# Kernel optimization log

Hardware: AMD Instinct MI355X
Metric: run time of the kernel (lower is better)

The kernel has to match this reference:

```python
import jax, jax.numpy as jnp
import numpy as np

B, L = 2, 256
H, W = 256, 128
FLAT = H * W              # 32768
D_MODEL = 1024
D_INNER = 2 * D_MODEL     # 2048
D_STATE = 16
D_CONV = 4
DT_RANK = D_MODEL // 16   # 64


def _rmsnorm(x, w, eps=1e-5):
    return x * jax.lax.rsqrt(jnp.mean(x * x, axis=-1, keepdims=True) + eps) * w


def _selective_scan(dA, dBu, C):
    # dA, dBu: (B, L, D_INNER, D_STATE); C: (B, L, D_STATE)
    def step(h, inp):
        a, bu, c = inp
        h = a * h + bu
        return h, jnp.einsum('bdn,bn->bd', h, c)
    h0 = jnp.zeros((dA.shape[0], dA.shape[2], dA.shape[3]), dA.dtype)
    _, ys = jax.lax.scan(step, h0, (jnp.swapaxes(dA, 0, 1), jnp.swapaxes(dBu, 0, 1), jnp.swapaxes(C, 0, 1)))
    return jnp.swapaxes(ys, 0, 1)  # (B, L, D_INNER)


def _mamba_block(x, norm_w, in_proj_w, conv_w, conv_b, x_proj_w, dt_proj_w, dt_proj_b, A_log, D_skip, out_proj_w):
    xn = _rmsnorm(x, norm_w)
    xz = xn @ in_proj_w.T                        # (B, L, 2*D_INNER)
    u, z = jnp.split(xz, 2, axis=-1)
    # causal depthwise conv over the sequence dim
    u = jax.lax.conv_general_dilated(u, conv_w, (1,), [(D_CONV - 1, 0)],
                                     dimension_numbers=('NWC', 'WIO', 'NWC'),
                                     feature_group_count=D_INNER) + conv_b
    u = jax.nn.silu(u)
    dbc = u @ x_proj_w.T                         # (B, L, DT_RANK + 2*D_STATE)
    dt_r, Bm, Cm = jnp.split(dbc, [DT_RANK, DT_RANK + D_STATE], axis=-1)
    dt = jax.nn.softplus(dt_r @ dt_proj_w.T + dt_proj_b)  # (B, L, D_INNER)
    A = -jnp.exp(A_log)                          # (D_INNER, D_STATE)
    dA = jnp.exp(dt[..., None] * A)              # (B, L, D_INNER, D_STATE)
    dBu = (dt * u)[..., None] * Bm[:, :, None, :]
    y = _selective_scan(dA, dBu, Cm) + D_skip * u
    y = y * jax.nn.silu(z)
    return x + y @ out_proj_w.T


def setup_inputs():
    key = jax.random.key(0)
    ks = jax.random.split(key, 12)
    g = lambda i, shape, sc: jax.random.normal(ks[i], shape, dtype=jnp.float32) * sc
    return {
        'x': (jax.random.uniform(ks[0], (B, L, H, W)) < 0.1).astype(jnp.float32),
        'enc_w': g(1, (D_MODEL, FLAT), 0.005),
        'enc_b': jnp.zeros((D_MODEL,), jnp.float32),
        'dec_w': g(2, (FLAT, D_MODEL), 0.02),
        'dec_b': jnp.zeros((FLAT,), jnp.float32),
        'norm_w': jnp.ones((D_MODEL,), jnp.float32),
        'in_proj_w': g(3, (2 * D_INNER, D_MODEL), 0.02),
        'conv_w': g(4, (D_CONV, 1, D_INNER), 0.2),
        'conv_b': jnp.zeros((D_INNER,), jnp.float32),
        'x_proj_w': g(5, (DT_RANK + 2 * D_STATE, D_INNER), 0.02),
        'dt_proj_w': g(6, (D_INNER, DT_RANK), 0.1),
        'dt_proj_b': jnp.full((D_INNER,), -2.0, jnp.float32),
        'A_log': jnp.log(jnp.tile(jnp.arange(1, D_STATE + 1, dtype=jnp.float32), (D_INNER, 1))),
        'D_skip': jnp.ones((D_INNER,), jnp.float32),
        'out_proj_w': g(7, (D_MODEL, D_INNER), 0.02),
    }


def reference(x, enc_w, enc_b, dec_w, dec_b, norm_w, in_proj_w, conv_w, conv_b,
              x_proj_w, dt_proj_w, dt_proj_b, A_log, D_skip, out_proj_w):
    b, l = x.shape[:2]
    lat = x.reshape(b, l, FLAT) @ enc_w.T + enc_b          # frozen encoder
    h = _mamba_block(lat, norm_w, in_proj_w, conv_w, conv_b, x_proj_w,
                     dt_proj_w, dt_proj_b, A_log, D_skip, out_proj_w)
    probs = jax.nn.sigmoid(h @ dec_w.T + dec_b)            # frozen decoder + sigmoid
    return probs.reshape(b, l, H, W)[:, :-1]
```

## Files before the change

### kernel.cpp

```cpp
#include <hip/hip_runtime.h>
#include <math.h>
#include <stdint.h>

#define BB 2
#define LL 256
#define FLAT 32768
#define DM 1024
#define DI 2048
#define DS 16
#define DTR 64
#define ML (BB*LL)

#define EPI_NONE 0
#define EPI_BIAS 1
#define EPI_SOFTPLUS 2
#define EPI_DEC 4

typedef __attribute__((ext_vector_type(8))) short bf16x8;
typedef __attribute__((ext_vector_type(4))) float f32x4;
typedef __attribute__((ext_vector_type(8))) unsigned short u16x8;
typedef __attribute__((ext_vector_type(4))) unsigned short u16x4;

__device__ __forceinline__ float sigmoid_f(float x) { return 1.0f / (1.0f + __expf(-x)); }

__device__ __forceinline__ unsigned short f2bf(float f) {
    unsigned u = __float_as_uint(f);
    u += 0x7fffu + ((u >> 16) & 1u);
    return (unsigned short)(u >> 16);
}

__device__ __forceinline__ unsigned cvt_pk_bf16(float a, float b) {
    unsigned r;
    asm("v_cvt_pk_bf16_f32 %0, %1, %2" : "=v"(r) : "v"(a), "v"(b));
    return r;
}

__device__ __forceinline__ void gld_lds16(const void* g, void* l) {
    __builtin_amdgcn_global_load_lds(
        (const __attribute__((address_space(1))) unsigned int*)g,
        (__attribute__((address_space(3))) unsigned int*)l, 16, 0, 0);
}

__global__ __launch_bounds__(256) void cvt_bf16_k(
    const float* __restrict__ in, unsigned short* __restrict__ out, int n8)
{
    const int i = blockIdx.x * 256 + threadIdx.x;
    if (i >= n8) return;
    const float4 a = ((const float4*)in)[2 * i];
    const float4 b = ((const float4*)in)[2 * i + 1];
    u16x8 r;
    r[0] = f2bf(a.x); r[1] = f2bf(a.y); r[2] = f2bf(a.z); r[3] = f2bf(a.w);
    r[4] = f2bf(b.x); r[5] = f2bf(b.y); r[6] = f2bf(b.z); r[7] = f2bf(b.w);
    ((u16x8*)out)[i] = r;
}

template<int EPI, bool SPLIT>
__global__ __launch_bounds__(256) void gemm_db(
    const unsigned short* __restrict__ A, const unsigned short* __restrict__ B,
    float* __restrict__ C, int M, int N, int K, int lda, int ldb, int kChunk,
    const float* __restrict__ bias)
{
    __shared__ __align__(16) char lds[65536];

    const int t  = threadIdx.x;
    const int w  = t >> 6;
    const int l  = t & 63;
    const int m0 = blockIdx.x * 128;
    const int n0 = blockIdx.y * 128;
    const int wr = w >> 1, wc = w & 1;

    int kb = 0, ke = K;
    float* Cout = C;
    if (SPLIT) { kb = blockIdx.z * kChunk; ke = kb + kChunk;
                 Cout = C + (size_t)blockIdx.z * M * N; }

    const int srow0 = w * 32 + (l >> 3);
    const int ssub  = l & 7;

    f32x4 acc[4][4];
#pragma unroll
    for (int i = 0; i < 4; ++i)
#pragma unroll
        for (int j = 0; j < 4; ++j) acc[i][j] = (f32x4){0.f, 0.f, 0.f, 0.f};

    const int lr = l & 15, h = l >> 4;

    auto STAGE = [&](int p, int kt) {
#pragma unroll
        for (int q = 0; q < 4; ++q) {
            const int row = srow0 + q * 8;
            gld_lds16(A + (size_t)(m0 + row) * lda + kt + ((ssub ^ (row & 7)) << 3),
                      lds + p * 32768 + w * 4096 + q * 1024);
        }
#pragma unroll
        for (int q = 0; q < 4; ++q) {
            const int row = srow0 + q * 8;
            gld_lds16(B + (size_t)(n0 + row) * ldb + kt + ((ssub ^ (row & 7)) << 3),
                      lds + p * 32768 + 16384 + w * 4096 + q * 1024);
        }
    };

    STAGE(0, kb);
    asm volatile("s_waitcnt vmcnt(0)" ::: "memory");
    __builtin_amdgcn_s_barrier();

    const int nt = (ke - kb) >> 6;
    int cur = 0;
    for (int tt = 0; tt < nt; ++tt) {
        if (tt + 1 < nt) STAGE(cur ^ 1, kb + ((tt + 1) << 6));
        const char* la = lds + cur * 32768;
        const char* lb = la + 16384;
#pragma unroll
        for (int ks = 0; ks < 2; ++ks) {
            bf16x8 af[4], bfr[4];
#pragma unroll
            for (int i = 0; i < 4; ++i) {
                const int r = wr * 64 + i * 16 + lr;
                const int sub = (ks * 4 + h) ^ (r & 7);
                af[i] = *(const bf16x8*)(la + r * 128 + sub * 16);
            }
#pragma unroll
            for (int j = 0; j < 4; ++j) {
                const int c = wc * 64 + j * 16 + lr;
                const int sub = (ks * 4 + h) ^ (c & 7);
                bfr[j] = *(const bf16x8*)(lb + c * 128 + sub * 16);
            }
#pragma unroll
            for (int i = 0; i < 4; ++i)
#pragma unroll
                for (int j = 0; j < 4; ++j)
                    acc[i][j] = __builtin_amdgcn_mfma_f32_16x16x32_bf16(
                        af[i], bfr[j], acc[i][j], 0, 0, 0);
        }
        asm volatile("s_waitcnt vmcnt(0)" ::: "memory");
        __builtin_amdgcn_s_barrier();
        cur ^= 1;
    }

#pragma unroll
    for (int i = 0; i < 4; ++i)
#pragma unroll
        for (int j = 0; j < 4; ++j)
#pragma unroll
            for (int rg = 0; rg < 4; ++rg) {
                const int row = m0 + wr * 64 + i * 16 + h * 4 + rg;
                const int col = n0 + wc * 64 + j * 16 + lr;
                float v = acc[i][j][rg];
                if (SPLIT || EPI == EPI_NONE) {
                    Cout[(size_t)row * N + col] = v;
                } else if (EPI == EPI_DEC) {
                    v = sigmoid_f(v + bias[col]);
                    const int b = row >> 8, ll = row & 255;
                    if (ll < 255) Cout[(((size_t)(b * 255 + ll)) << 15) + col] = v;
                }
            }
}

template<int EPI, bool SPLIT, bool BF32>
__global__ __launch_bounds__(256) void gemm_bf16(
    const unsigned short* __restrict__ A, const void* __restrict__ Bv,
    float* __restrict__ C, int M, int N, int K, int lda, int ldb, int kChunk,
    const float* __restrict__ bias)
{
    __shared__ __align__(16) char lds[BF32 ? 49152 : 32768];

    const float*          Bf = (const float*)Bv;
    const unsigned short* Bh = (const unsigned short*)Bv;

    const int t  = threadIdx.x;
    const int w  = t >> 6;
    const int l  = t & 63;
    const int m0 = blockIdx.x * 128;
    const int n0 = blockIdx.y * 128;
    const int wr = w >> 1, wc = w & 1;

    int kb = 0, ke = K;
    float* Cout = C;
    if (SPLIT) { kb = blockIdx.z * kChunk; ke = kb + kChunk;
                 Cout = C + (size_t)blockIdx.z * M * N; }

    const int srow0 = w * 32 + (l >> 3);
    const int ssub  = l & 7;
    const int brow0 = w * 32 + (l >> 4);
    const int bgl   = l & 15;

    f32x4 acc[4][4];
#pragma unroll
    for (int i = 0; i < 4; ++i)
#pragma unroll
        for (int j = 0; j < 4; ++j) acc[i][j] = (f32x4){0.f, 0.f, 0.f, 0.f};

    const int lr = l & 15, h = l >> 4;

    for (int kt = kb; kt < ke; kt += 64) {
#pragma unroll
        for (int q = 0; q < 4; ++q) {
            const int row = srow0 + q * 8;
            gld_lds16(A + (size_t)(m0 + row) * lda + kt + ((ssub ^ (row & 7)) << 3),
                      lds + w * 4096 + q * 1024);
        }
        if (BF32) {
#pragma unroll
            for (int q = 0; q < 8; ++q) {
                const int row = brow0 + q * 4;
                gld_lds16(Bf + (size_t)(n0 + row) * ldb + kt + ((bgl ^ (row & 15)) << 2),
                          lds + 16384 + w * 8192 + q * 1024);
            }
        } else {
#pragma unroll
            for (int q = 0; q < 4; ++q) {
                const int row = srow0 + q * 8;
                gld_lds16(Bh + (size_t)(n0 + row) * ldb + kt + ((ssub ^ (row & 7)) << 3),
                          lds + 16384 + w * 4096 + q * 1024);
            }
        }
        __syncthreads();

#pragma unroll
        for (int ks = 0; ks < 2; ++ks) {
            bf16x8 af[4], bfr[4];
#pragma unroll
            for (int i = 0; i < 4; ++i) {
                const int r = wr * 64 + i * 16 + lr;
                const int sub = (ks * 4 + h) ^ (r & 7);
                af[i] = *(const bf16x8*)(lds + r * 128 + sub * 16);
            }
#pragma unroll
            for (int j = 0; j < 4; ++j) {
                const int c = wc * 64 + j * 16 + lr;
                if (BF32) {
                    const int g0 = (2 * (ks * 4 + h))     ^ (c & 15);
                    const int g1 = (2 * (ks * 4 + h) + 1) ^ (c & 15);
                    const f32x4 v0 = *(const f32x4*)(lds + 16384 + c * 256 + g0 * 16);
                    const f32x4 v1 = *(const f32x4*)(lds + 16384 + c * 256 + g1 * 16);
                    union { unsigned u[4]; bf16x8 v; } cv;
                    cv.u[0] = cvt_pk_bf16(v0[0], v0[1]);
                    cv.u[1] = cvt_pk_bf16(v0[2], v0[3]);
                    cv.u[2] = cvt_pk_bf16(v1[0], v1[1]);
                    cv.u[3] = cvt_pk_bf16(v1[2], v1[3]);
                    bfr[j] = cv.v;
                } else {
                    const int sub = (ks * 4 + h) ^ (c & 7);
                    bfr[j] = *(const bf16x8*)(lds + 16384 + c * 128 + sub * 16);
                }
            }
#pragma unroll
            for (int i = 0; i < 4; ++i)
#pragma unroll
                for (int j = 0; j < 4; ++j)
                    acc[i][j] = __builtin_amdgcn_mfma_f32_16x16x32_bf16(
                        af[i], bfr[j], acc[i][j], 0, 0, 0);
        }
        __syncthreads();
    }

#pragma unroll
    for (int i = 0; i < 4; ++i)
#pragma unroll
        for (int j = 0; j < 4; ++j)
#pragma unroll
            for (int rg = 0; rg < 4; ++rg) {
                const int row = m0 + wr * 64 + i * 16 + h * 4 + rg;
                const int col = n0 + wc * 64 + j * 16 + lr;
                float v = acc[i][j][rg];
                if (SPLIT || EPI == EPI_NONE) {
                    Cout[(size_t)row * N + col] = v;
                } else if (EPI == EPI_DEC) {
                    v = sigmoid_f(v + bias[col]);
                    const int b = row >> 8, ll = row & 255;
                    if (ll < 255) Cout[(((size_t)(b * 255 + ll)) << 15) + col] = v;
                }
            }
}

template<int EPI, bool SPLIT>
__global__ __launch_bounds__(256) void gemm_nt(
    const float* __restrict__ A, const float* __restrict__ B,
    float* __restrict__ C, int M, int N, int K, int lda, int ldb,
    int kChunk, const float* __restrict__ bias)
{
    __shared__ float As[32][64];
    __shared__ float Bs[32][64];

    const int m0 = blockIdx.x * 64;
    const int n0 = blockIdx.y * 64;
    const int t  = threadIdx.x;

    int kb = 0, ke = K;
    float* Cout = C;
    if (SPLIT) { kb = blockIdx.z * kChunk; ke = kb + kChunk; Cout = C + (size_t)blockIdx.z * M * N; }

    const int lrow = t >> 3;
    const int lcol = (t & 7) << 2;

    float acc[4][4];
#pragma unroll
    for (int i = 0; i < 4; ++i)
#pragma unroll
        for (int j = 0; j < 4; ++j) acc[i][j] = 0.0f;

    const int tx = t & 15, ty = t >> 4;

    for (int k = kb; k < ke; k += 32) {
#pragma unroll
        for (int i = 0; i < 2; ++i) {
            const int row = lrow + i * 32;
            float4 av = *(const float4*)&A[(m0 + row) * lda + k + lcol];
            As[lcol + 0][row] = av.x; As[lcol + 1][row] = av.y;
            As[lcol + 2][row] = av.z; As[lcol + 3][row] = av.w;
            const int nn = n0 + row;
            float4 bv = make_float4(0.f, 0.f, 0.f, 0.f);
            if (nn < N) bv = *(const float4*)&B[nn * ldb + k + lcol];
            Bs[lcol + 0][row] = bv.x; Bs[lcol + 1][row] = bv.y;
            Bs[lcol + 2][row] = bv.z; Bs[lcol + 3][row] = bv.w;
        }
        __syncthreads();
#pragma unroll
        for (int kk = 0; kk < 32; ++kk) {
            float4 a4 = *(const float4*)&As[kk][ty << 2];
            float4 b4 = *(const float4*)&Bs[kk][tx << 2];
            const float a[4] = { a4.x, a4.y, a4.z, a4.w };
            const float b[4] = { b4.x, b4.y, b4.z, b4.w };
#pragma unroll
            for (int i = 0; i < 4; ++i)
#pragma unroll
                for (int j = 0; j < 4; ++j)
                    acc[i][j] = fmaf(a[i], b[j], acc[i][j]);
        }
        __syncthreads();
    }

#pragma unroll
    for (int i = 0; i < 4; ++i) {
        const int m = m0 + (ty << 2) + i;
#pragma unroll
        for (int j = 0; j < 4; ++j) {
            const int n = n0 + (tx << 2) + j;
            if (n >= N) continue;
            float v = acc[i][j];
            if (SPLIT || EPI == EPI_NONE) {
                Cout[m * N + n] = v;
            } else if (EPI == EPI_SOFTPLUS) {
                v += bias[n];
                Cout[m * N + n] = fmaxf(v, 0.0f) + log1pf(__expf(-fabsf(v)));
            }
        }
    }
}

template<int EPI>
__global__ __launch_bounds__(256) void splitk_reduce(
    const float* __restrict__ part, float* __restrict__ C,
    int MN, int N, int S, const float* __restrict__ bias)
{
    const int i = blockIdx.x * 256 + threadIdx.x;
    if (i >= MN) return;
    float s = 0.0f;
    for (int j = 0; j < S; ++j) s += part[(size_t)j * MN + i];
    if (EPI == EPI_BIAS) s += bias[i % N];
    C[i] = s;
}

__global__ __launch_bounds__(256) void splitk_reduce_resid_bf16(
    const float* __restrict__ part, const float* __restrict__ resid,
    unsigned short* __restrict__ outb, int MN, int S)
{
    const int i = blockIdx.x * 256 + threadIdx.x;
    if (i >= MN) return;
    float s = 0.0f;
    for (int j = 0; j < S; ++j) s += part[(size_t)j * MN + i];
    outb[i] = f2bf(s + resid[i]);
}

__global__ __launch_bounds__(256) void rmsnorm_k(
    const float* __restrict__ x, const float* __restrict__ w,
    unsigned short* __restrict__ o)
{
    const int row = blockIdx.x;
    const int t = threadIdx.x;
    const float* xr = x + row * DM;
    float4 xv = *(const float4*)&xr[t * 4];
    float ss = xv.x * xv.x + xv.y * xv.y + xv.z * xv.z + xv.w * xv.w;
#pragma unroll
    for (int off = 32; off > 0; off >>= 1) ss += __shfl_xor(ss, off);
    __shared__ float red[4];
    if ((t & 63) == 0) red[t >> 6] = ss;
    __syncthreads();
    const float tot = red[0] + red[1] + red[2] + red[3];
    const float scale = rsqrtf(tot * (1.0f / DM) + 1e-5f);
    float4 wv = *(const float4*)&w[t * 4];
    u16x4 ov;
    ov[0] = f2bf(xv.x * scale * wv.x); ov[1] = f2bf(xv.y * scale * wv.y);
    ov[2] = f2bf(xv.z * scale * wv.z); ov[3] = f2bf(xv.w * scale * wv.w);
    *(u16x4*)&o[row * DM + t * 4] = ov;
}

__global__ __launch_bounds__(256) void conv_silu_k(
    const float* __restrict__ xz, const float* __restrict__ cw,
    const float* __restrict__ cb, float* __restrict__ u)
{
    const int idx = blockIdx.x * 256 + threadIdx.x;
    if (idx >= ML * DI) return;
    const int d  = idx & (DI - 1);
    const int bl = idx >> 11;
    const int l  = bl & (LL - 1);
    float s = cb[d];
#pragma unroll
    for (int w = 0; w < 4; ++w) {
        const int ls = l - 3 + w;
        if (ls >= 0) s = fmaf(xz[(bl - 3 + w) * (2 * DI) + d], cw[w * DI + d], s);
    }
    u[idx] = s * sigmoid_f(s);
}

__global__ __launch_bounds__(256) void scan_k(
    const float* __restrict__ dt, const float* __restrict__ u,
    const float* __restrict__ xz, const float* __restrict__ dbc,
    const float* __restrict__ A_log, const float* __restrict__ Dskip,
    unsigned short* __restrict__ y)
{
    const int t = blockIdx.x * 256 + threadIdx.x;
    const int n  = t & (DS - 1);
    const int ch = t >> 4;
    const int d  = ch & (DI - 1);
    const int b  = ch >> 11;
    const float a  = -__expf(A_log[d * DS + n]);
    const float Dv = Dskip[d];
    float h = 0.0f;
    const int rbase = b * LL;

    for (int l0 = 0; l0 < LL; l0 += 8) {
        float dtv[8], uv[8], Bv[8], Cv[8], zv[8];
#pragma unroll
        for (int s = 0; s < 8; ++s) {
            const int r = rbase + l0 + s;
            dtv[s] = dt[r * DI + d];
            uv[s]  = u[r * DI + d];
            Bv[s]  = dbc[r * 96 + DTR + n];
            Cv[s]  = dbc[r * 96 + DTR + DS + n];
            zv[s]  = xz[r * (2 * DI) + DI + d];
        }
        float p[8];
#pragma unroll
        for (int s = 0; s < 8; ++s) {
            const float dA = __expf(dtv[s] * a);
            h = fmaf(dA, h, dtv[s] * uv[s] * Bv[s]);
            p[s] = h * Cv[s];
        }
#pragma unroll
        for (int s = 0; s < 8; ++s) p[s] += __shfl_xor(p[s], 1);
#pragma unroll
        for (int s = 0; s < 8; ++s) p[s] += __shfl_xor(p[s], 2);
#pragma unroll
        for (int s = 0; s < 8; ++s) p[s] += __shfl_xor(p[s], 4);
#pragma unroll
        for (int s = 0; s < 8; ++s) p[s] += __shfl_xor(p[s], 8);
        if (n == 0) {
#pragma unroll
            for (int s = 0; s < 8; ++s) {
                const int r = rbase + l0 + s;
                const float yy = fmaf(Dv, uv[s], p[s]);
                y[r * DI + d] = f2bf(yy * zv[s] * sigmoid_f(zv[s]));
            }
        }
    }
}

extern "C" void kernel_launch(void* const* d_in, const int* in_sizes, int n_in,
                              void* d_out, int out_size, void* d_ws, size_t ws_size,
                              hipStream_t stream)
{
    const float* x        = (const float*)d_in[0];
    const float* enc_w    = (const float*)d_in[1];
    const float* enc_b    = (const float*)d_in[2];
    const float* dec_w    = (const float*)d_in[3];
    const float* dec_b    = (const float*)d_in[4];
    const float* norm_w   = (const float*)d_in[5];
    const float* in_proj  = (const float*)d_in[6];
    const float* conv_w   = (const float*)d_in[7];
    const float* conv_b   = (const float*)d_in[8];
    const float* x_proj   = (const float*)d_in[9];
    const float* dt_projw = (const float*)d_in[10];
    const float* dt_projb = (const float*)d_in[11];
    const float* A_log    = (const float*)d_in[12];
    const float* D_skip   = (const float*)d_in[13];
    const float* out_proj = (const float*)d_in[14];
    float* out = (float*)d_out;
    (void)in_sizes; (void)n_in; (void)out_size; (void)ws_size;

    char* wsb = (char*)d_ws;
    unsigned short* wbf = (unsigned short*)(wsb);
    float* part = (float*)(wsb + 67108864);
    float* lat  = (float*)(wsb + 100663296);
    float* dt   = (float*)(wsb + 102760448);
    char* S0 = wsb + 106954752;
    unsigned short* xbf    = (unsigned short*)(S0);
    unsigned short* xnbf   = (unsigned short*)(S0);
    unsigned short* ybf    = (unsigned short*)(S0 + 1048576);
    unsigned short* houtbf = (unsigned short*)(S0 + 3145728);
    float* xz  = (float*)(S0 + 4194304);
    float* u   = (float*)(S0 + 12582912);
    float* dbc = (float*)(S0 + 16777216);

    cvt_bf16_k<<<(FLAT * ML / 8) / 256, 256, 0, stream>>>(x, xbf, FLAT * ML / 8);
    cvt_bf16_k<<<(DM * FLAT / 8) / 256, 256, 0, stream>>>(enc_w, wbf, DM * FLAT / 8);

    {
        dim3 g(ML / 128, DM / 128, 16);
        gemm_db<EPI_NONE, true><<<g, 256, 0, stream>>>(
            xbf, wbf, part, ML, DM, FLAT, FLAT, FLAT, FLAT / 16, nullptr);
        splitk_reduce<EPI_BIAS><<<(ML * DM) / 256, 256, 0, stream>>>(part, lat, ML * DM, DM, 16, enc_b);
    }

    rmsnorm_k<<<ML, 256, 0, stream>>>(lat, norm_w, xnbf);

    {
        dim3 g(ML / 128, (2 * DI) / 128);
        gemm_bf16<EPI_NONE, false, true><<<g, 256, 0, stream>>>(
            xnbf, in_proj, xz, ML, 2 * DI, DM, DM, DM, 0, nullptr);
    }

    conv_silu_k<<<(ML * DI) / 256, 256, 0, stream>>>(xz, conv_w, conv_b, u);

    {
        dim3 g(ML / 64, 2, 16);
        gemm_nt<EPI_NONE, true><<<g, 256, 0, stream>>>(u, x_proj, part, ML, 96, DI, DI, DI,
                                                       DI / 16, nullptr);
        splitk_reduce<EPI_NONE><<<(ML * 96 + 255) / 256, 256, 0, stream>>>(part, dbc, ML * 96, 96, 16, nullptr);
    }

    {
        dim3 g(ML / 64, DI / 64);
        gemm_nt<EPI_SOFTPLUS, false><<<g, 256, 0, stream>>>(dbc, dt_projw, dt, ML, DI, DTR,
                                                            96, DTR, 0, dt_projb);
    }

    scan_k<<<(BB * DI * DS) / 256, 256, 0, stream>>>(dt, u, xz, dbc, A_log, D_skip, ybf);

    {
        dim3 g(ML / 128, DM / 128, 8);
        gemm_bf16<EPI_NONE, true, true><<<g, 256, 0, stream>>>(
            ybf, out_proj, part, ML, DM, DI, DI, DI, DI / 8, nullptr);
        splitk_reduce_resid_bf16<<<(ML * DM) / 256, 256, 0, stream>>>(part, lat, houtbf, ML * DM, 8);
    }

    cvt_bf16_k<<<(FLAT * DM / 8) / 256, 256, 0, stream>>>(dec_w, wbf, FLAT * DM / 8);
    {
        dim3 g(ML / 128, FLAT / 128);
        gemm_db<EPI_DEC, false><<<g, 256, 0, stream>>>(
            houtbf, wbf, out, ML, FLAT, DM, DM, DM, 0, dec_b);
    }
}
```

Measured before the change: 633.5 us.

## Fuse fp32-to-bf16 weight conversion into GEMM staging and merge reduce with RMSNorm

The encoder and decoder GEMMs now load fp32 weights straight into registers, convert them to bf16, and write them to LDS inside the pipelined loop. This removes the two separate conversion passes over the 32M-element weight matrices, which wrote and reread a bf16 copy. The split-K reduction, encoder bias and RMSNorm are also merged into one kernel. In exchange, the GEMMs read twice as many weight bytes, and the weight path now goes through registers instead of direct-to-LDS loads, which adds VGPR pressure and conversion ALU work.

```diff
diff --git a/kernel.cpp b/kernel.cpp
--- a/kernel.cpp
+++ b/kernel.cpp
@@ -55,8 +55,8 @@
 }
 
 template<int EPI, bool SPLIT>
-__global__ __launch_bounds__(256) void gemm_db(
-    const unsigned short* __restrict__ A, const unsigned short* __restrict__ B,
+__global__ __launch_bounds__(256) void gemm_db2(
+    const unsigned short* __restrict__ A, const float* __restrict__ Bf,
     float* __restrict__ C, int M, int N, int K, int lda, int ldb, int kChunk,
     const float* __restrict__ bias)
 {
@@ -85,29 +85,52 @@
 
     const int lr = l & 15, h = l >> 4;
 
-    auto STAGE = [&](int p, int kt) {
+    float4 breg[4][2];
+
+    auto STAGE_A = [&](int p, int kt) {
 #pragma unroll
         for (int q = 0; q < 4; ++q) {
             const int row = srow0 + q * 8;
             gld_lds16(A + (size_t)(m0 + row) * lda + kt + ((ssub ^ (row & 7)) << 3),
                       lds + p * 32768 + w * 4096 + q * 1024);
         }
+    };
+    auto LOAD_B = [&](int kt) {
 #pragma unroll
         for (int q = 0; q < 4; ++q) {
             const int row = srow0 + q * 8;
-            gld_lds16(B + (size_t)(n0 + row) * ldb + kt + ((ssub ^ (row & 7)) << 3),
-                      lds + p * 32768 + 16384 + w * 4096 + q * 1024);
+            const int G = ssub ^ (row & 7);
+            const float4* src = (const float4*)&Bf[(size_t)(n0 + row) * ldb + kt + G * 8];
+            breg[q][0] = src[0];
+            breg[q][1] = src[1];
         }
     };
-
-    STAGE(0, kb);
-    asm volatile("s_waitcnt vmcnt(0)" ::: "memory");
-    __builtin_amdgcn_s_barrier();
+    auto WRITE_B = [&](int p) {
+#pragma unroll
+        for (int q = 0; q < 4; ++q) {
+            const int row = srow0 + q * 8;
+            union { unsigned u[4]; bf16x8 v; } cv;
+            cv.u[0] = cvt_pk_bf16(breg[q][0].x, breg[q][0].y);
+            cv.u[1] = cvt_pk_bf16(breg[q][0].z, breg[q][0].w);
+            cv.u[2] = cvt_pk_bf16(breg[q][1].x, breg[q][1].y);
+            cv.u[3] = cvt_pk_bf16(breg[q][1].z, breg[q][1].w);
+            *(bf16x8*)(lds + p * 32768 + 16384 + row * 128 + ssub * 16) = cv.v;
+        }
+    };
+
+    STAGE_A(0, kb);
+    LOAD_B(kb);
+    WRITE_B(0);
+    __syncthreads();
 
     const int nt = (ke - kb) >> 6;
     int cur = 0;
     for (int tt = 0; tt < nt; ++tt) {
-        if (tt + 1 < nt) STAGE(cur ^ 1, kb + ((tt + 1) << 6));
+        if (tt + 1 < nt) {
+            const int ktn = kb + ((tt + 1) << 6);
+            STAGE_A(cur ^ 1, ktn);
+            LOAD_B(ktn);
+        }
         const char* la = lds + cur * 32768;
         const char* lb = la + 16384;
 #pragma unroll
@@ -132,8 +155,8 @@
                     acc[i][j] = __builtin_amdgcn_mfma_f32_16x16x32_bf16(
                         af[i], bfr[j], acc[i][j], 0, 0, 0);
         }
-        asm volatile("s_waitcnt vmcnt(0)" ::: "memory");
-        __builtin_amdgcn_s_barrier();
+        if (tt + 1 < nt) WRITE_B(cur ^ 1);
+        __syncthreads();
         cur ^= 1;
     }
 
@@ -372,15 +395,24 @@
     outb[i] = f2bf(s + resid[i]);
 }
 
-__global__ __launch_bounds__(256) void rmsnorm_k(
-    const float* __restrict__ x, const float* __restrict__ w,
-    unsigned short* __restrict__ o)
+__global__ __launch_bounds__(256) void reduce_rms_k(
+    const float* __restrict__ part, const float* __restrict__ bias,
+    const float* __restrict__ w, float* __restrict__ lat,
+    unsigned short* __restrict__ xn, int S)
 {
     const int row = blockIdx.x;
     const int t = threadIdx.x;
-    const float* xr = x + row * DM;
-    float4 xv = *(const float4*)&xr[t * 4];
-    float ss = xv.x * xv.x + xv.y * xv.y + xv.z * xv.z + xv.w * xv.w;
+    const float* p = part + (size_t)row * DM + t * 4;
+    float4 s = make_float4(0.f, 0.f, 0.f, 0.f);
+    for (int j = 0; j < S; ++j) {
+        const float4 v = *(const float4*)(p + (size_t)j * (ML * DM));
+        s.x += v.x; s.y += v.y; s.z += v.z; s.w += v.w;
+    }
+    const float4 bv = *(const float4*)&bias[t * 4];
+    s.x += bv.x; s.y += bv.y; s.z += bv.z; s.w += bv.w;
+    *(float4*)&lat[(size_t)row * DM + t * 4] = s;
+
+    float ss = s.x * s.x + s.y * s.y + s.z * s.z + s.w * s.w;
 #pragma unroll
     for (int off = 32; off > 0; off >>= 1) ss += __shfl_xor(ss, off);
     __shared__ float red[4];
@@ -388,11 +420,11 @@
     __syncthreads();
     const float tot = red[0] + red[1] + red[2] + red[3];
     const float scale = rsqrtf(tot * (1.0f / DM) + 1e-5f);
-    float4 wv = *(const float4*)&w[t * 4];
+    const float4 wv = *(const float4*)&w[t * 4];
     u16x4 ov;
-    ov[0] = f2bf(xv.x * scale * wv.x); ov[1] = f2bf(xv.y * scale * wv.y);
-    ov[2] = f2bf(xv.z * scale * wv.z); ov[3] = f2bf(xv.w * scale * wv.w);
-    *(u16x4*)&o[row * DM + t * 4] = ov;
+    ov[0] = f2bf(s.x * scale * wv.x); ov[1] = f2bf(s.y * scale * wv.y);
+    ov[2] = f2bf(s.z * scale * wv.z); ov[3] = f2bf(s.w * scale * wv.w);
+    *(u16x4*)&xn[(size_t)row * DM + t * 4] = ov;
 }
 
 __global__ __launch_bounds__(256) void conv_silu_k(
@@ -489,11 +521,10 @@
     (void)in_sizes; (void)n_in; (void)out_size; (void)ws_size;
 
     char* wsb = (char*)d_ws;
-    unsigned short* wbf = (unsigned short*)(wsb);
-    float* part = (float*)(wsb + 67108864);
-    float* lat  = (float*)(wsb + 100663296);
-    float* dt   = (float*)(wsb + 102760448);
-    char* S0 = wsb + 106954752;
+    float* part = (float*)(wsb);
+    float* lat  = (float*)(wsb + 33554432);
+    float* dt   = (float*)(wsb + 35651584);
+    char* S0 = wsb + 41943040;
     unsigned short* xbf    = (unsigned short*)(S0);
     unsigned short* xnbf   = (unsigned short*)(S0);
     unsigned short* ybf    = (unsigned short*)(S0 + 1048576);
@@ -503,16 +534,13 @@
     float* dbc = (float*)(S0 + 16777216);
 
     cvt_bf16_k<<<(FLAT * ML / 8) / 256, 256, 0, stream>>>(x, xbf, FLAT * ML / 8);
-    cvt_bf16_k<<<(DM * FLAT / 8) / 256, 256, 0, stream>>>(enc_w, wbf, DM * FLAT / 8);
 
     {
         dim3 g(ML / 128, DM / 128, 16);
-        gemm_db<EPI_NONE, true><<<g, 256, 0, stream>>>(
-            xbf, wbf, part, ML, DM, FLAT, FLAT, FLAT, FLAT / 16, nullptr);
-        splitk_reduce<EPI_BIAS><<<(ML * DM) / 256, 256, 0, stream>>>(part, lat, ML * DM, DM, 16, enc_b);
-    }
-
-    rmsnorm_k<<<ML, 256, 0, stream>>>(lat, norm_w, xnbf);
+        gemm_db2<EPI_NONE, true><<<g, 256, 0, stream>>>(
+            xbf, enc_w, part, ML, DM, FLAT, FLAT, FLAT, FLAT / 16, nullptr);
+    }
+    reduce_rms_k<<<ML, 256, 0, stream>>>(part, enc_b, norm_w, lat, xnbf, 16);
 
     {
         dim3 g(ML / 128, (2 * DI) / 128);
@@ -544,10 +572,9 @@
         splitk_reduce_resid_bf16<<<(ML * DM) / 256, 256, 0, stream>>>(part, lat, houtbf, ML * DM, 8);
     }
 
-    cvt_bf16_k<<<(FLAT * DM / 8) / 256, 256, 0, stream>>>(dec_w, wbf, FLAT * DM / 8);
     {
         dim3 g(ML / 128, FLAT / 128);
-        gemm_db<EPI_DEC, false><<<g, 256, 0, stream>>>(
-            houtbf, wbf, out, ML, FLAT, DM, DM, DM, 0, dec_b);
-    }
-}
+        gemm_db2<EPI_DEC, false><<<g, 256, 0, stream>>>(
+            houtbf, dec_w, out, ML, FLAT, DM, DM, DM, 0, dec_b);
+    }
+}
```

Measured after the change: 624.2 us. About the same (-1.5%).
